# Performance work log

Hardware: AMD Instinct MI355X
Metric: run time of the kernel (lower is better)

The kernel has to match this reference:

```python
import jax, jax.numpy as jnp
import numpy as np

B, N, FD, H = 8, 256, 1024, 256
RATIO, TEMP = 0.6, 0.5


def setup_inputs() -> dict:
    key = jax.random.key(0)
    ks = jax.random.split(key, 5)
    x = jax.random.normal(ks[0], (B, N, FD), dtype=jnp.float32)
    s1 = 1.0 / np.sqrt(2 * FD)
    W1 = jax.random.uniform(ks[1], (H, 2 * FD), minval=-s1, maxval=s1, dtype=jnp.float32)
    b1 = jax.random.uniform(ks[2], (H,), minval=-s1, maxval=s1, dtype=jnp.float32)
    s2 = 1.0 / np.sqrt(H)
    W2 = jax.random.uniform(ks[3], (1, H), minval=-s2, maxval=s2, dtype=jnp.float32)
    b2 = jax.random.uniform(ks[4], (1,), minval=-s2, maxval=s2, dtype=jnp.float32)
    return {"x": x, "W1": W1, "b1": b1, "W2": W2, "b2": b2}


def reference(x, W1, b1, W2, b2):
    Bb, Nn, Fd = x.shape
    # Linear on cat([row, col]) == row @ W1[:, :F].T + col @ W1[:, F:].T + b1,
    # so project nodes once and broadcast-add instead of materializing [N,N,2F].
    pr = jnp.einsum('bnf,hf->bnh', x, W1[:, :Fd])  # row projections
    pc = jnp.einsum('bnf,hf->bnh', x, W1[:, Fd:])  # col projections
    h = jax.nn.relu(pr[:, :, None, :] + pc[:, None, :, :] + b1)  # [B,N,N,H]
    edge_scores = jnp.einsum('bijh,h->bij', h, W2[0]) + b2[0]    # [B,N,N]
    flat = edge_scores.reshape(Bb, Nn * Nn)
    soft_mask = jax.nn.softmax(flat / TEMP, axis=1)
    k = int(RATIO * Nn * Nn)
    topk_vals, _ = jax.lax.top_k(soft_mask, k)
    threshold = topk_vals[:, -1:]
    causal_mask = jnp.where(soft_mask >= threshold, soft_mask, jnp.zeros_like(soft_mask))
    causal_mask = causal_mask / (causal_mask.sum(axis=1, keepdims=True) + 1e-12)
    conf_mask = 1.0 - causal_mask
    causal_adj = causal_mask.reshape(Bb, Nn, Nn)
    conf_adj = conf_mask.reshape(Bb, Nn, Nn)
    return (causal_adj, conf_adj, edge_scores, soft_mask)
```

## Files before the change

### kernel.cpp

```cpp
#include <hip/hip_runtime.h>

#define BB 8
#define NN 256
#define FDIM 1024
#define HDIM 256
#define NSQ 65536
#define ROWS 2048
#define KSEL 39321

typedef short s16x8 __attribute__((ext_vector_type(8)));
typedef float f32x4 __attribute__((ext_vector_type(4)));

__device__ __forceinline__ unsigned fkey(float f) {
  unsigned u = __float_as_uint(f);
  return (u & 0x80000000u) ? ~u : (u | 0x80000000u);
}
__device__ __forceinline__ float finv(unsigned k) {
  unsigned u = (k & 0x80000000u) ? (k & 0x7fffffffu) : ~k;
  return __uint_as_float(u);
}
__device__ __forceinline__ unsigned short f2bf(float f) {
  unsigned u = __float_as_uint(f);
  unsigned r = (u + 0x7fffu + ((u >> 16) & 1u)) >> 16;
  return (unsigned short)r;
}

#define NZERO 131080
__global__ __launch_bounds__(256) void k_init(unsigned* __restrict__ z) {
  int idx = blockIdx.x * 256 + threadIdx.x;
  if (idx < NZERO) z[idx] = 0u;
}

#define LDSW 72
__global__ __launch_bounds__(256) void k_gemm(const float* __restrict__ X,
                                              const float* __restrict__ W1,
                                              const float* __restrict__ b1,
                                              float* __restrict__ PRBT,
                                              float* __restrict__ PCT) {
  const int bm = blockIdx.x * 64;
  const int bn = blockIdx.y * 64;
  const int t = threadIdx.x;
  __shared__ short As[64 * LDSW];
  __shared__ short Bs[64 * LDSW];
  const int sr = t >> 2, cg = t & 3;
  const float* pa = X + (bm + sr) * FDIM + cg * 16;
  const float* pb = (bn < 256) ? (W1 + (bn + sr) * (2 * FDIM) + cg * 16)
                               : (W1 + (bn - 256 + sr) * (2 * FDIM) + FDIM + cg * 16);
  const int w = t >> 6, lane = t & 63;
  const int wm = (w >> 1) * 32, wn = (w & 1) * 32;
  const int q = lane >> 4, m16 = lane & 15;
  f32x4 acc[2][2] = {};
  for (int k0 = 0; k0 < FDIM; k0 += 64) {
    float4 a0 = *(const float4*)(pa + k0);
    float4 a1 = *(const float4*)(pa + k0 + 4);
    float4 a2 = *(const float4*)(pa + k0 + 8);
    float4 a3 = *(const float4*)(pa + k0 + 12);
    float4 b0 = *(const float4*)(pb + k0);
    float4 b1v = *(const float4*)(pb + k0 + 4);
    float4 b2v = *(const float4*)(pb + k0 + 8);
    float4 b3v = *(const float4*)(pb + k0 + 12);
    s16x8 avlo, avhi, bvlo, bvhi;
    avlo[0] = (short)f2bf(a0.x); avlo[1] = (short)f2bf(a0.y); avlo[2] = (short)f2bf(a0.z); avlo[3] = (short)f2bf(a0.w);
    avlo[4] = (short)f2bf(a1.x); avlo[5] = (short)f2bf(a1.y); avlo[6] = (short)f2bf(a1.z); avlo[7] = (short)f2bf(a1.w);
    avhi[0] = (short)f2bf(a2.x); avhi[1] = (short)f2bf(a2.y); avhi[2] = (short)f2bf(a2.z); avhi[3] = (short)f2bf(a2.w);
    avhi[4] = (short)f2bf(a3.x); avhi[5] = (short)f2bf(a3.y); avhi[6] = (short)f2bf(a3.z); avhi[7] = (short)f2bf(a3.w);
    bvlo[0] = (short)f2bf(b0.x); bvlo[1] = (short)f2bf(b0.y); bvlo[2] = (short)f2bf(b0.z); bvlo[3] = (short)f2bf(b0.w);
    bvlo[4] = (short)f2bf(b1v.x); bvlo[5] = (short)f2bf(b1v.y); bvlo[6] = (short)f2bf(b1v.z); bvlo[7] = (short)f2bf(b1v.w);
    bvhi[0] = (short)f2bf(b2v.x); bvhi[1] = (short)f2bf(b2v.y); bvhi[2] = (short)f2bf(b2v.z); bvhi[3] = (short)f2bf(b2v.w);
    bvhi[4] = (short)f2bf(b3v.x); bvhi[5] = (short)f2bf(b3v.y); bvhi[6] = (short)f2bf(b3v.z); bvhi[7] = (short)f2bf(b3v.w);
    __syncthreads();
    *(s16x8*)&As[sr * LDSW + cg * 16]     = avlo;
    *(s16x8*)&As[sr * LDSW + cg * 16 + 8] = avhi;
    *(s16x8*)&Bs[sr * LDSW + cg * 16]     = bvlo;
    *(s16x8*)&Bs[sr * LDSW + cg * 16 + 8] = bvhi;
    __syncthreads();
    {
      s16x8 af0 = *(s16x8*)&As[(wm + m16) * LDSW + q * 8];
      s16x8 af1 = *(s16x8*)&As[(wm + 16 + m16) * LDSW + q * 8];
      s16x8 bf0 = *(s16x8*)&Bs[(wn + m16) * LDSW + q * 8];
      s16x8 bf1 = *(s16x8*)&Bs[(wn + 16 + m16) * LDSW + q * 8];
      acc[0][0] = __builtin_amdgcn_mfma_f32_16x16x32_bf16(af0, bf0, acc[0][0], 0, 0, 0);
      acc[0][1] = __builtin_amdgcn_mfma_f32_16x16x32_bf16(af0, bf1, acc[0][1], 0, 0, 0);
      acc[1][0] = __builtin_amdgcn_mfma_f32_16x16x32_bf16(af1, bf0, acc[1][0], 0, 0, 0);
      acc[1][1] = __builtin_amdgcn_mfma_f32_16x16x32_bf16(af1, bf1, acc[1][1], 0, 0, 0);
    }
    {
      s16x8 af0 = *(s16x8*)&As[(wm + m16) * LDSW + 32 + q * 8];
      s16x8 af1 = *(s16x8*)&As[(wm + 16 + m16) * LDSW + 32 + q * 8];
      s16x8 bf0 = *(s16x8*)&Bs[(wn + m16) * LDSW + 32 + q * 8];
      s16x8 bf1 = *(s16x8*)&Bs[(wn + 16 + m16) * LDSW + 32 + q * 8];
      acc[0][0] = __builtin_amdgcn_mfma_f32_16x16x32_bf16(af0, bf0, acc[0][0], 0, 0, 0);
      acc[0][1] = __builtin_amdgcn_mfma_f32_16x16x32_bf16(af0, bf1, acc[0][1], 0, 0, 0);
      acc[1][0] = __builtin_amdgcn_mfma_f32_16x16x32_bf16(af1, bf0, acc[1][0], 0, 0, 0);
      acc[1][1] = __builtin_amdgcn_mfma_f32_16x16x32_bf16(af1, bf1, acc[1][1], 0, 0, 0);
    }
  }
#pragma unroll
  for (int rt = 0; rt < 2; ++rt) {
#pragma unroll
    for (int ct = 0; ct < 2; ++ct) {
      const int hn = bn + wn + ct * 16 + m16;
      const int row0 = bm + wm + rt * 16 + q * 4;
      if (hn < 256) {
        const float bias = b1[hn];
        float4 v = make_float4(acc[rt][ct][0] + bias, acc[rt][ct][1] + bias,
                               acc[rt][ct][2] + bias, acc[rt][ct][3] + bias);
        *(float4*)&PRBT[hn * ROWS + row0] = v;
      } else {
        float4 v = make_float4(acc[rt][ct][0], acc[rt][ct][1],
                               acc[rt][ct][2], acc[rt][ct][3]);
        *(float4*)&PCT[(hn - 256) * ROWS + row0] = v;
      }
    }
  }
}

__global__ __launch_bounds__(256) void k_edge(const float* __restrict__ PRBT,
                                              const float* __restrict__ PCT,
                                              const float* __restrict__ W2,
                                              const float* __restrict__ b2,
                                              float* __restrict__ edge,
                                              float* __restrict__ sumE,
                                              unsigned* __restrict__ hist1,
                                              float* __restrict__ vsum1) {
  const int b = blockIdx.z;
  const int i0 = blockIdx.y * 64, j0 = blockIdx.x * 32;
  const int t = threadIdx.x;
  __shared__ float prs[64][68];
  __shared__ float pcs[64][36];
  __shared__ float w2s[HDIM];
  __shared__ unsigned lh[4096];
  __shared__ float lhv[4096];
  __shared__ float wm[4];
  w2s[t] = W2[t];
#pragma unroll
  for (int i = 0; i < 16; ++i) { lh[t + i * 256] = 0u; lhv[t + i * 256] = 0.f; }
  const float bias = b2[0];
  const int tmi = t >> 4, tnj = t & 15;
  float acc[4][2] = {};
  for (int h0 = 0; h0 < HDIM; h0 += 64) {
    __syncthreads();
#pragma unroll
    for (int it = 0; it < 4; ++it) {
      int hh = it * 16 + (t >> 4);
      int ig = t & 15;
      *(float4*)&prs[hh][ig * 4] =
          *(const float4*)&PRBT[(h0 + hh) * ROWS + b * NN + i0 + ig * 4];
    }
#pragma unroll
    for (int it = 0; it < 2; ++it) {
      int hh = it * 32 + (t >> 3);
      int jg = t & 7;
      *(float4*)&pcs[hh][jg * 4] =
          *(const float4*)&PCT[(h0 + hh) * ROWS + b * NN + j0 + jg * 4];
    }
    __syncthreads();
#pragma unroll 8
    for (int h = 0; h < 64; ++h) {
      const float w = w2s[h0 + h];
      const float4 a = *(const float4*)&prs[h][tmi * 4];
      const float2 c = *(const float2*)&pcs[h][tnj * 2];
      const float ai[4] = {a.x, a.y, a.z, a.w};
#pragma unroll
      for (int i = 0; i < 4; ++i) {
        acc[i][0] += fmaxf(ai[i] + c.x, 0.f) * w;
        acc[i][1] += fmaxf(ai[i] + c.y, 0.f) * w;
      }
    }
  }
  float s = 0.f;
  const int ibase = i0 + tmi * 4, jbase = j0 + tnj * 2;
#pragma unroll
  for (int i = 0; i < 4; ++i) {
    float2 v = make_float2(acc[i][0] + bias, acc[i][1] + bias);
    *(float2*)&edge[b * NSQ + (ibase + i) * NN + jbase] = v;
    float ex = __expf(v.x * 2.f), ey = __expf(v.y * 2.f);
    s += ex + ey;
    unsigned bx = fkey(v.x) >> 20, by = fkey(v.y) >> 20;
    atomicAdd(&lh[bx], 1u);  atomicAdd(&lhv[bx], ex);
    atomicAdd(&lh[by], 1u);  atomicAdd(&lhv[by], ey);
  }
  for (int off = 32; off > 0; off >>= 1) s += __shfl_down(s, off);
  if ((t & 63) == 0) wm[t >> 6] = s;
  __syncthreads();
  if (t == 0) atomicAdd(&sumE[b], wm[0] + wm[1] + wm[2] + wm[3]);
  unsigned* g = hist1 + b * 4096;
  float* gv = vsum1 + b * 4096;
#pragma unroll
  for (int i = 0; i < 16; ++i) {
    unsigned c = lh[t + i * 256];
    if (c) { atomicAdd(&g[t + i * 256], c); atomicAdd(&gv[t + i * 256], lhv[t + i * 256]); }
  }
}

__device__ __forceinline__ void scan_pair(const unsigned* __restrict__ hc,
                                          const float* __restrict__ hv, int k,
                                          unsigned* S, float* V,
                                          unsigned* ou, float* of,
                                          unsigned& bin, int& kres,
                                          float& vabove, float& vbin) {
  const int t = threadIdx.x;
  unsigned loc[16]; float locv[16];
  unsigned cs = 0; float vs = 0.f;
#pragma unroll
  for (int i = 0; i < 16; ++i) {
    loc[i] = hc[t * 16 + i]; cs += loc[i];
    locv[i] = hv[t * 16 + i]; vs += locv[i];
  }
  S[t] = cs; V[t] = vs;
  __syncthreads();
  for (int off = 1; off < 256; off <<= 1) {
    unsigned su = (t + off < 256) ? S[t + off] : 0u;
    float vu = (t + off < 256) ? V[t + off] : 0.f;
    __syncthreads();
    S[t] += su; V[t] += vu;
    __syncthreads();
  }
  const int above = (int)(S[t] - cs);
  if (above < k && (int)S[t] >= k) {
    int cum = above;
    float vcum = V[t] - vs;
    for (int i = 15; i >= 0; --i) {
      cum += (int)loc[i];
      if (cum >= k) {
        ou[0] = (unsigned)(t * 16 + i);
        ou[1] = (unsigned)(k - (cum - (int)loc[i]));
        of[0] = vcum;
        of[1] = locv[i];
        break;
      }
      vcum += locv[i];
    }
  }
  __syncthreads();
  bin = ou[0]; kres = (int)ou[1]; vabove = of[0]; vbin = of[1];
  __syncthreads();
}

__global__ __launch_bounds__(256) void k_hist2(const float* __restrict__ edge,
                                               const unsigned* __restrict__ hist1,
                                               const float* __restrict__ vsum1,
                                               unsigned* __restrict__ hist2,
                                               float* __restrict__ vsum2) {
  const int b = blockIdx.y;
  const int t = threadIdx.x;
  __shared__ unsigned S[256];
  __shared__ float V[256];
  __shared__ unsigned ou[2];
  __shared__ float of[2];
  __shared__ unsigned lh[4096];
  __shared__ float lhv[4096];
#pragma unroll
  for (int i = 0; i < 16; ++i) { lh[t + i * 256] = 0u; lhv[t + i * 256] = 0.f; }
  unsigned p1; int k2; float va, vb;
  scan_pair(hist1 + b * 4096, vsum1 + b * 4096, KSEL, S, V, ou, of, p1, k2, va, vb);
  const float* p = edge + b * NSQ + blockIdx.x * 2048 + t * 8;
#pragma unroll
  for (int i = 0; i < 8; i += 4) {
    float4 v = *(const float4*)&p[i];
    unsigned kx = fkey(v.x), ky = fkey(v.y), kz = fkey(v.z), kw = fkey(v.w);
    if ((kx >> 20) == p1) { atomicAdd(&lh[(kx >> 8) & 0xFFFu], 1u); atomicAdd(&lhv[(kx >> 8) & 0xFFFu], __expf(v.x * 2.f)); }
    if ((ky >> 20) == p1) { atomicAdd(&lh[(ky >> 8) & 0xFFFu], 1u); atomicAdd(&lhv[(ky >> 8) & 0xFFFu], __expf(v.y * 2.f)); }
    if ((kz >> 20) == p1) { atomicAdd(&lh[(kz >> 8) & 0xFFFu], 1u); atomicAdd(&lhv[(kz >> 8) & 0xFFFu], __expf(v.z * 2.f)); }
    if ((kw >> 20) == p1) { atomicAdd(&lh[(kw >> 8) & 0xFFFu], 1u); atomicAdd(&lhv[(kw >> 8) & 0xFFFu], __expf(v.w * 2.f)); }
  }
  __syncthreads();
  unsigned* g = hist2 + b * 4096;
  float* gv = vsum2 + b * 4096;
#pragma unroll
  for (int i = 0; i < 16; ++i) {
    unsigned c = lh[t + i * 256];
    if (c) { atomicAdd(&g[t + i * 256], c); atomicAdd(&gv[t + i * 256], lhv[t + i * 256]); }
  }
}

__global__ __launch_bounds__(256) void k_out(const float* __restrict__ edge,
                                             const float* __restrict__ sumE,
                                             const unsigned* __restrict__ hist1,
                                             const float* __restrict__ vsum1,
                                             const unsigned* __restrict__ hist2,
                                             const float* __restrict__ vsum2,
                                             float* __restrict__ soft,
                                             float* __restrict__ causal,
                                             float* __restrict__ conf) {
  const int b = blockIdx.y;
  const int t = threadIdx.x;
  __shared__ unsigned S[256];
  __shared__ float V[256];
  __shared__ unsigned ou[2];
  __shared__ float of[2];
  unsigned p1, p2; int k2, k3;
  float va1, vb1, va2, vb2;
  scan_pair(hist1 + b * 4096, vsum1 + b * 4096, KSEL, S, V, ou, of, p1, k2, va1, vb1);
  scan_pair(hist2 + b * 4096, vsum2 + b * 4096, k2, S, V, ou, of, p2, k3, va2, vb2);
  const float th = finv((p1 << 20) | (p2 << 8));
  const float Z = sumE[b];
  const float invZ = 1.f / Z;
  const float msum = (va1 + va2 + vb2) * invZ;
  const float invD = 1.f / (msum + 1e-12f);
  const int off = b * NSQ + blockIdx.x * 2048 + t * 8;
#pragma unroll
  for (int i = 0; i < 8; i += 4) {
    float4 v = *(const float4*)&edge[off + i];
    float4 o = make_float4(__expf(v.x * 2.f) * invZ, __expf(v.y * 2.f) * invZ,
                           __expf(v.z * 2.f) * invZ, __expf(v.w * 2.f) * invZ);
    *(float4*)&soft[off + i] = o;
    float cx = v.x >= th ? o.x * invD : 0.f;
    float cy = v.y >= th ? o.y * invD : 0.f;
    float cz = v.z >= th ? o.z * invD : 0.f;
    float cw = v.w >= th ? o.w * invD : 0.f;
    *(float4*)&causal[off + i] = make_float4(cx, cy, cz, cw);
    *(float4*)&conf[off + i]   = make_float4(1.f - cx, 1.f - cy, 1.f - cz, 1.f - cw);
  }
}

extern "C" void kernel_launch(void* const* d_in, const int* in_sizes, int n_in,
                              void* d_out, int out_size, void* d_ws, size_t ws_size,
                              hipStream_t stream) {
  const float* x  = (const float*)d_in[0];
  const float* W1 = (const float*)d_in[1];
  const float* b1 = (const float*)d_in[2];
  const float* W2 = (const float*)d_in[3];
  const float* b2 = (const float*)d_in[4];

  float* out = (float*)d_out;
  float* causal = out;
  float* conf   = out + 1 * 524288;
  float* edge   = out + 2 * 524288;
  float* soft   = out + 3 * 524288;

  float* ws = (float*)d_ws;
  float*    PRBT  = ws;
  float*    PCT   = ws + 524288;
  unsigned* base  = (unsigned*)(ws + 1048576);
  unsigned* hist1 = base;
  float*    vsum1 = (float*)(base + 32768);
  unsigned* hist2 = base + 65536;
  float*    vsum2 = (float*)(base + 98304);
  float*    sumE  = (float*)(base + 131072);

  k_init<<<(NZERO + 255) / 256, 256, 0, stream>>>(base);
  k_gemm<<<dim3(32, 8), 256, 0, stream>>>(x, W1, b1, PRBT, PCT);
  k_edge<<<dim3(8, 4, 8), 256, 0, stream>>>(PRBT, PCT, W2, b2, edge, sumE, hist1, vsum1);
  k_hist2<<<dim3(32, 8), 256, 0, stream>>>(edge, hist1, vsum1, hist2, vsum2);
  k_out<<<dim3(32, 8), 256, 0, stream>>>(edge, sumE, hist1, vsum1, hist2, vsum2,
                                         soft, causal, conf);
}
```

Baseline: 126.5 us.

## Replace two-pass radix top-k with single 14-bit histogram and pre-convert bf16

The two-level 12+12-bit histogram threshold search (k_edge histogram plus separate k_hist2 pass) becomes a single 14-bit-key histogram with packed 16-bit counts in LDS. The threshold is now the bin boundary, and the softmax normalizer comes from the histogram value sums. That removes one kernel and the extra read of edge scores. A new prep kernel converts X and W1 to bf16 once and zeroes the histograms, so the GEMM loads half the bytes and does no conversion. This risks an inexact top-k threshold when several values share the boundary bin (the coarser binning collapses ties). It also adds more global atomics for the larger histogram and more serial scanning work in k_out.

```diff
diff --git a/kernel.cpp b/kernel.cpp
--- a/kernel.cpp
+++ b/kernel.cpp
@@ -7,6 +7,7 @@
 #define NSQ 65536
 #define ROWS 2048
 #define KSEL 39321
+#define NBIN 16384
 
 typedef short s16x8 __attribute__((ext_vector_type(8)));
 typedef float f32x4 __attribute__((ext_vector_type(4)));
@@ -25,15 +26,31 @@
   return (unsigned short)r;
 }
 
-#define NZERO 131080
-__global__ __launch_bounds__(256) void k_init(unsigned* __restrict__ z) {
-  int idx = blockIdx.x * 256 + threadIdx.x;
-  if (idx < NZERO) z[idx] = 0u;
+__global__ __launch_bounds__(256) void k_prep(const float* __restrict__ X,
+                                              const float* __restrict__ W1,
+                                              unsigned short* __restrict__ XB,
+                                              unsigned short* __restrict__ W1B,
+                                              unsigned* __restrict__ zero) {
+  const int bx = blockIdx.x, t = threadIdx.x;
+  if (bx < 1280) {
+    const float* src = (bx < 1024) ? X : W1;
+    unsigned short* dst = (bx < 1024) ? XB : W1B;
+    const int idx = ((bx < 1024 ? bx : bx - 1024) * 256 + t) * 8;
+    float4 v0 = *(const float4*)&src[idx];
+    float4 v1 = *(const float4*)&src[idx + 4];
+    s16x8 o;
+    o[0] = (short)f2bf(v0.x); o[1] = (short)f2bf(v0.y); o[2] = (short)f2bf(v0.z); o[3] = (short)f2bf(v0.w);
+    o[4] = (short)f2bf(v1.x); o[5] = (short)f2bf(v1.y); o[6] = (short)f2bf(v1.z); o[7] = (short)f2bf(v1.w);
+    *(s16x8*)&dst[idx] = o;
+  } else {
+    const int idx = ((bx - 1280) * 256 + t) * 4;
+    *(uint4*)&zero[idx] = make_uint4(0u, 0u, 0u, 0u);
+  }
 }
 
 #define LDSW 72
-__global__ __launch_bounds__(256) void k_gemm(const float* __restrict__ X,
-                                              const float* __restrict__ W1,
+__global__ __launch_bounds__(256) void k_gemm(const unsigned short* __restrict__ XB,
+                                              const unsigned short* __restrict__ W1B,
                                               const float* __restrict__ b1,
                                               float* __restrict__ PRBT,
                                               float* __restrict__ PCT) {
@@ -43,36 +60,24 @@
   __shared__ short As[64 * LDSW];
   __shared__ short Bs[64 * LDSW];
   const int sr = t >> 2, cg = t & 3;
-  const float* pa = X + (bm + sr) * FDIM + cg * 16;
-  const float* pb = (bn < 256) ? (W1 + (bn + sr) * (2 * FDIM) + cg * 16)
-                               : (W1 + (bn - 256 + sr) * (2 * FDIM) + FDIM + cg * 16);
+  const unsigned short* pa = XB + (bm + sr) * FDIM + cg * 16;
+  const unsigned short* pb = (bn < 256)
+      ? (W1B + (bn + sr) * (2 * FDIM) + cg * 16)
+      : (W1B + (bn - 256 + sr) * (2 * FDIM) + FDIM + cg * 16);
   const int w = t >> 6, lane = t & 63;
   const int wm = (w >> 1) * 32, wn = (w & 1) * 32;
   const int q = lane >> 4, m16 = lane & 15;
   f32x4 acc[2][2] = {};
   for (int k0 = 0; k0 < FDIM; k0 += 64) {
-    float4 a0 = *(const float4*)(pa + k0);
-    float4 a1 = *(const float4*)(pa + k0 + 4);
-    float4 a2 = *(const float4*)(pa + k0 + 8);
-    float4 a3 = *(const float4*)(pa + k0 + 12);
-    float4 b0 = *(const float4*)(pb + k0);
-    float4 b1v = *(const float4*)(pb + k0 + 4);
-    float4 b2v = *(const float4*)(pb + k0 + 8);
-    float4 b3v = *(const float4*)(pb + k0 + 12);
-    s16x8 avlo, avhi, bvlo, bvhi;
-    avlo[0] = (short)f2bf(a0.x); avlo[1] = (short)f2bf(a0.y); avlo[2] = (short)f2bf(a0.z); avlo[3] = (short)f2bf(a0.w);
-    avlo[4] = (short)f2bf(a1.x); avlo[5] = (short)f2bf(a1.y); avlo[6] = (short)f2bf(a1.z); avlo[7] = (short)f2bf(a1.w);
-    avhi[0] = (short)f2bf(a2.x); avhi[1] = (short)f2bf(a2.y); avhi[2] = (short)f2bf(a2.z); avhi[3] = (short)f2bf(a2.w);
-    avhi[4] = (short)f2bf(a3.x); avhi[5] = (short)f2bf(a3.y); avhi[6] = (short)f2bf(a3.z); avhi[7] = (short)f2bf(a3.w);
-    bvlo[0] = (short)f2bf(b0.x); bvlo[1] = (short)f2bf(b0.y); bvlo[2] = (short)f2bf(b0.z); bvlo[3] = (short)f2bf(b0.w);
-    bvlo[4] = (short)f2bf(b1v.x); bvlo[5] = (short)f2bf(b1v.y); bvlo[6] = (short)f2bf(b1v.z); bvlo[7] = (short)f2bf(b1v.w);
-    bvhi[0] = (short)f2bf(b2v.x); bvhi[1] = (short)f2bf(b2v.y); bvhi[2] = (short)f2bf(b2v.z); bvhi[3] = (short)f2bf(b2v.w);
-    bvhi[4] = (short)f2bf(b3v.x); bvhi[5] = (short)f2bf(b3v.y); bvhi[6] = (short)f2bf(b3v.z); bvhi[7] = (short)f2bf(b3v.w);
-    __syncthreads();
-    *(s16x8*)&As[sr * LDSW + cg * 16]     = avlo;
-    *(s16x8*)&As[sr * LDSW + cg * 16 + 8] = avhi;
-    *(s16x8*)&Bs[sr * LDSW + cg * 16]     = bvlo;
-    *(s16x8*)&Bs[sr * LDSW + cg * 16 + 8] = bvhi;
+    s16x8 a0 = *(const s16x8*)(pa + k0);
+    s16x8 a1 = *(const s16x8*)(pa + k0 + 8);
+    s16x8 b0 = *(const s16x8*)(pb + k0);
+    s16x8 b1v = *(const s16x8*)(pb + k0 + 8);
+    __syncthreads();
+    *(s16x8*)&As[sr * LDSW + cg * 16]     = a0;
+    *(s16x8*)&As[sr * LDSW + cg * 16 + 8] = a1;
+    *(s16x8*)&Bs[sr * LDSW + cg * 16]     = b0;
+    *(s16x8*)&Bs[sr * LDSW + cg * 16 + 8] = b1v;
     __syncthreads();
     {
       s16x8 af0 = *(s16x8*)&As[(wm + m16) * LDSW + q * 8];
@@ -120,21 +125,21 @@
                                               const float* __restrict__ W2,
                                               const float* __restrict__ b2,
                                               float* __restrict__ edge,
-                                              float* __restrict__ sumE,
-                                              unsigned* __restrict__ hist1,
-                                              float* __restrict__ vsum1) {
+                                              unsigned* __restrict__ gcount,
+                                              float* __restrict__ gvsum) {
   const int b = blockIdx.z;
   const int i0 = blockIdx.y * 64, j0 = blockIdx.x * 32;
   const int t = threadIdx.x;
   __shared__ float prs[64][68];
   __shared__ float pcs[64][36];
   __shared__ float w2s[HDIM];
-  __shared__ unsigned lh[4096];
-  __shared__ float lhv[4096];
-  __shared__ float wm[4];
+  __shared__ unsigned lhc[NBIN / 2];
+  __shared__ float lhv[NBIN];
   w2s[t] = W2[t];
 #pragma unroll
-  for (int i = 0; i < 16; ++i) { lh[t + i * 256] = 0u; lhv[t + i * 256] = 0.f; }
+  for (int i = 0; i < 8; ++i) ((uint4*)lhc)[t + i * 256] = make_uint4(0u, 0u, 0u, 0u);
+#pragma unroll
+  for (int i = 0; i < 16; ++i) ((float4*)lhv)[t + i * 256] = make_float4(0.f, 0.f, 0.f, 0.f);
   const float bias = b2[0];
   const int tmi = t >> 4, tnj = t & 15;
   float acc[4][2] = {};
@@ -168,118 +173,42 @@
       }
     }
   }
-  float s = 0.f;
   const int ibase = i0 + tmi * 4, jbase = j0 + tnj * 2;
 #pragma unroll
   for (int i = 0; i < 4; ++i) {
     float2 v = make_float2(acc[i][0] + bias, acc[i][1] + bias);
     *(float2*)&edge[b * NSQ + (ibase + i) * NN + jbase] = v;
     float ex = __expf(v.x * 2.f), ey = __expf(v.y * 2.f);
-    s += ex + ey;
-    unsigned bx = fkey(v.x) >> 20, by = fkey(v.y) >> 20;
-    atomicAdd(&lh[bx], 1u);  atomicAdd(&lhv[bx], ex);
-    atomicAdd(&lh[by], 1u);  atomicAdd(&lhv[by], ey);
-  }
-  for (int off = 32; off > 0; off >>= 1) s += __shfl_down(s, off);
-  if ((t & 63) == 0) wm[t >> 6] = s;
+    unsigned bx = fkey(v.x) >> 18, by = fkey(v.y) >> 18;
+    atomicAdd(&lhc[bx >> 1], 1u << ((bx & 1) * 16));
+    atomicAdd(&lhv[bx], ex);
+    atomicAdd(&lhc[by >> 1], 1u << ((by & 1) * 16));
+    atomicAdd(&lhv[by], ey);
+  }
   __syncthreads();
-  if (t == 0) atomicAdd(&sumE[b], wm[0] + wm[1] + wm[2] + wm[3]);
-  unsigned* g = hist1 + b * 4096;
-  float* gv = vsum1 + b * 4096;
-#pragma unroll
-  for (int i = 0; i < 16; ++i) {
-    unsigned c = lh[t + i * 256];
-    if (c) { atomicAdd(&g[t + i * 256], c); atomicAdd(&gv[t + i * 256], lhv[t + i * 256]); }
-  }
-}
-
-__device__ __forceinline__ void scan_pair(const unsigned* __restrict__ hc,
-                                          const float* __restrict__ hv, int k,
-                                          unsigned* S, float* V,
-                                          unsigned* ou, float* of,
-                                          unsigned& bin, int& kres,
-                                          float& vabove, float& vbin) {
-  const int t = threadIdx.x;
-  unsigned loc[16]; float locv[16];
-  unsigned cs = 0; float vs = 0.f;
-#pragma unroll
-  for (int i = 0; i < 16; ++i) {
-    loc[i] = hc[t * 16 + i]; cs += loc[i];
-    locv[i] = hv[t * 16 + i]; vs += locv[i];
-  }
-  S[t] = cs; V[t] = vs;
-  __syncthreads();
-  for (int off = 1; off < 256; off <<= 1) {
-    unsigned su = (t + off < 256) ? S[t + off] : 0u;
-    float vu = (t + off < 256) ? V[t + off] : 0.f;
-    __syncthreads();
-    S[t] += su; V[t] += vu;
-    __syncthreads();
-  }
-  const int above = (int)(S[t] - cs);
-  if (above < k && (int)S[t] >= k) {
-    int cum = above;
-    float vcum = V[t] - vs;
-    for (int i = 15; i >= 0; --i) {
-      cum += (int)loc[i];
-      if (cum >= k) {
-        ou[0] = (unsigned)(t * 16 + i);
-        ou[1] = (unsigned)(k - (cum - (int)loc[i]));
-        of[0] = vcum;
-        of[1] = locv[i];
-        break;
-      }
-      vcum += locv[i];
-    }
-  }
-  __syncthreads();
-  bin = ou[0]; kres = (int)ou[1]; vabove = of[0]; vbin = of[1];
-  __syncthreads();
-}
-
-__global__ __launch_bounds__(256) void k_hist2(const float* __restrict__ edge,
-                                               const unsigned* __restrict__ hist1,
-                                               const float* __restrict__ vsum1,
-                                               unsigned* __restrict__ hist2,
-                                               float* __restrict__ vsum2) {
-  const int b = blockIdx.y;
-  const int t = threadIdx.x;
-  __shared__ unsigned S[256];
-  __shared__ float V[256];
-  __shared__ unsigned ou[2];
-  __shared__ float of[2];
-  __shared__ unsigned lh[4096];
-  __shared__ float lhv[4096];
-#pragma unroll
-  for (int i = 0; i < 16; ++i) { lh[t + i * 256] = 0u; lhv[t + i * 256] = 0.f; }
-  unsigned p1; int k2; float va, vb;
-  scan_pair(hist1 + b * 4096, vsum1 + b * 4096, KSEL, S, V, ou, of, p1, k2, va, vb);
-  const float* p = edge + b * NSQ + blockIdx.x * 2048 + t * 8;
-#pragma unroll
-  for (int i = 0; i < 8; i += 4) {
-    float4 v = *(const float4*)&p[i];
-    unsigned kx = fkey(v.x), ky = fkey(v.y), kz = fkey(v.z), kw = fkey(v.w);
-    if ((kx >> 20) == p1) { atomicAdd(&lh[(kx >> 8) & 0xFFFu], 1u); atomicAdd(&lhv[(kx >> 8) & 0xFFFu], __expf(v.x * 2.f)); }
-    if ((ky >> 20) == p1) { atomicAdd(&lh[(ky >> 8) & 0xFFFu], 1u); atomicAdd(&lhv[(ky >> 8) & 0xFFFu], __expf(v.y * 2.f)); }
-    if ((kz >> 20) == p1) { atomicAdd(&lh[(kz >> 8) & 0xFFFu], 1u); atomicAdd(&lhv[(kz >> 8) & 0xFFFu], __expf(v.z * 2.f)); }
-    if ((kw >> 20) == p1) { atomicAdd(&lh[(kw >> 8) & 0xFFFu], 1u); atomicAdd(&lhv[(kw >> 8) & 0xFFFu], __expf(v.w * 2.f)); }
-  }
-  __syncthreads();
-  unsigned* g = hist2 + b * 4096;
-  float* gv = vsum2 + b * 4096;
-#pragma unroll
-  for (int i = 0; i < 16; ++i) {
-    unsigned c = lh[t + i * 256];
-    if (c) { atomicAdd(&g[t + i * 256], c); atomicAdd(&gv[t + i * 256], lhv[t + i * 256]); }
+  unsigned* gc = gcount + b * NBIN;
+  float* gv = gvsum + b * NBIN;
+#pragma unroll
+  for (int i = 0; i < 32; ++i) {
+    const int idx = t + i * 256;
+    unsigned wv = lhc[idx];
+    if (wv) {
+      unsigned lo = wv & 0xFFFFu, hi = wv >> 16;
+      if (lo) atomicAdd(&gc[2 * idx], lo);
+      if (hi) atomicAdd(&gc[2 * idx + 1], hi);
+    }
+  }
+#pragma unroll
+  for (int i = 0; i < 64; ++i) {
+    const int idx = t + i * 256;
+    float vv = lhv[idx];
+    if (vv != 0.f) atomicAdd(&gv[idx], vv);
   }
 }
 
 __global__ __launch_bounds__(256) void k_out(const float* __restrict__ edge,
-                                             const float* __restrict__ sumE,
-                                             const unsigned* __restrict__ hist1,
-                                             const float* __restrict__ vsum1,
-                                             const unsigned* __restrict__ hist2,
-                                             const float* __restrict__ vsum2,
+                                             const unsigned* __restrict__ gcount,
+                                             const float* __restrict__ gvsum,
                                              float* __restrict__ soft,
                                              float* __restrict__ causal,
                                              float* __restrict__ conf) {
@@ -287,16 +216,39 @@
   const int t = threadIdx.x;
   __shared__ unsigned S[256];
   __shared__ float V[256];
-  __shared__ unsigned ou[2];
-  __shared__ float of[2];
-  unsigned p1, p2; int k2, k3;
-  float va1, vb1, va2, vb2;
-  scan_pair(hist1 + b * 4096, vsum1 + b * 4096, KSEL, S, V, ou, of, p1, k2, va1, vb1);
-  scan_pair(hist2 + b * 4096, vsum2 + b * 4096, k2, S, V, ou, of, p2, k3, va2, vb2);
-  const float th = finv((p1 << 20) | (p2 << 8));
-  const float Z = sumE[b];
+  __shared__ unsigned ou[1];
+  __shared__ float of[3];
+  const unsigned* hc = gcount + b * NBIN;
+  const float* hv = gvsum + b * NBIN;
+  unsigned cs = 0; float vs = 0.f;
+  for (int i = 0; i < 64; ++i) { cs += hc[t * 64 + i]; vs += hv[t * 64 + i]; }
+  S[t] = cs; V[t] = vs;
+  __syncthreads();
+  for (int off = 1; off < 256; off <<= 1) {
+    unsigned su = (t + off < 256) ? S[t + off] : 0u;
+    float vu = (t + off < 256) ? V[t + off] : 0.f;
+    __syncthreads();
+    S[t] += su; V[t] += vu;
+    __syncthreads();
+  }
+  if (t == 0) of[2] = V[0];
+  const int above = (int)(S[t] - cs);
+  if (above < KSEL && (int)S[t] >= KSEL) {
+    int cum = above;
+    float vcum = V[t] - vs;
+    for (int i = 63; i >= 0; --i) {
+      unsigned c = hc[t * 64 + i];
+      float v = hv[t * 64 + i];
+      cum += (int)c;
+      if (cum >= KSEL) { ou[0] = (unsigned)(t * 64 + i); of[0] = vcum; of[1] = v; break; }
+      vcum += v;
+    }
+  }
+  __syncthreads();
+  const float th = finv(ou[0] << 18);
+  const float Z = of[2];
   const float invZ = 1.f / Z;
-  const float msum = (va1 + va2 + vb2) * invZ;
+  const float msum = (of[0] + of[1]) * invZ;
   const float invD = 1.f / (msum + 1e-12f);
   const int off = b * NSQ + blockIdx.x * 2048 + t * 8;
 #pragma unroll
@@ -330,19 +282,15 @@
   float* soft   = out + 3 * 524288;
 
   float* ws = (float*)d_ws;
-  float*    PRBT  = ws;
-  float*    PCT   = ws + 524288;
-  unsigned* base  = (unsigned*)(ws + 1048576);
-  unsigned* hist1 = base;
-  float*    vsum1 = (float*)(base + 32768);
-  unsigned* hist2 = base + 65536;
-  float*    vsum2 = (float*)(base + 98304);
-  float*    sumE  = (float*)(base + 131072);
-
-  k_init<<<(NZERO + 255) / 256, 256, 0, stream>>>(base);
-  k_gemm<<<dim3(32, 8), 256, 0, stream>>>(x, W1, b1, PRBT, PCT);
-  k_edge<<<dim3(8, 4, 8), 256, 0, stream>>>(PRBT, PCT, W2, b2, edge, sumE, hist1, vsum1);
-  k_hist2<<<dim3(32, 8), 256, 0, stream>>>(edge, hist1, vsum1, hist2, vsum2);
-  k_out<<<dim3(32, 8), 256, 0, stream>>>(edge, sumE, hist1, vsum1, hist2, vsum2,
-                                         soft, causal, conf);
-}
+  float*          PRBT   = ws;
+  float*          PCT    = ws + 524288;
+  unsigned short* XB     = (unsigned short*)(ws + 1048576);
+  unsigned short* W1B    = (unsigned short*)(ws + 2097152);
+  unsigned*       gcount = (unsigned*)(ws + 2359296);
+  float*          gvsum  = (float*)(ws + 2490368);
+
+  k_prep<<<1536, 256, 0, stream>>>(x, W1, XB, W1B, gcount);
+  k_gemm<<<dim3(32, 8), 256, 0, stream>>>(XB, W1B, b1, PRBT, PCT);
+  k_edge<<<dim3(8, 4, 8), 256, 0, stream>>>(PRBT, PCT, W2, b2, edge, gcount, gvsum);
+  k_out<<<dim3(32, 8), 256, 0, stream>>>(edge, gcount, gvsum, soft, causal, conf);
+}
```

After: 120.4 us. 1.05x faster.
